# Performance work log

Hardware: AMD Instinct MI355X
Metric: run time of the kernel (lower is better)

The kernel has to match this reference:

```python
import jax, jax.numpy as jnp
import numpy as np

N = 50000      # nodes
E = 800000     # edges (avg degree 16)
F_IN = 128     # num_node_features
D = 64         # embedding_size (= per-head out_channels)
H = 4          # heads
ED = 20        # edge_dim (hardcoded in module)
SLOPE = 0.2    # GATv2 leaky_relu negative slope
N_LAYERS = 3   # conv applied 3 times with shared weights


def setup_inputs() -> dict:
    key = jax.random.key(0)
    ks = jax.random.split(key, 12)
    s = 0.1
    return {
        "x": jax.random.normal(ks[0], (N, F_IN), jnp.float32),
        "edge_attr": jax.random.normal(ks[1], (E, 2), jnp.float32),
        "edge_index": jax.random.randint(ks[2], (2, E), 0, N, dtype=jnp.int32),
        # f: Linear(F_IN, D)
        "f_W": jax.random.normal(ks[3], (F_IN, D), jnp.float32) * s,
        "f_b": jnp.zeros((D,), jnp.float32),
        # fe: Linear(2, ED)
        "fe_W": jax.random.normal(ks[4], (2, ED), jnp.float32) * s,
        "fe_b": jnp.zeros((ED,), jnp.float32),
        # GATv2Conv lin_l / lin_r: Linear(D, H*D)
        "Wl": jax.random.normal(ks[5], (D, H * D), jnp.float32) * s,
        "bl": jnp.zeros((H * D,), jnp.float32),
        "Wr": jax.random.normal(ks[6], (D, H * D), jnp.float32) * s,
        "br": jnp.zeros((H * D,), jnp.float32),
        # lin_edge: Linear(ED, H*D, bias=False)
        "We": jax.random.normal(ks[7], (ED, H * D), jnp.float32) * s,
        # attention vector att: [H, D]
        "att": jax.random.normal(ks[8], (H, D), jnp.float32) * s,
        # final bias (concat=False -> size D)
        "bias": jnp.zeros((D,), jnp.float32),
    }


def _gatv2_conv(h, e_emb, src, dst, Wl, bl, Wr, br, We, att, bias):
    # h: [N, D], e_emb: [E, ED], src/dst: [E]
    xl = (h @ Wl + bl).reshape(-1, H, D)        # source transform  [N,H,D]
    xr = (h @ Wr + br).reshape(-1, H, D)        # target transform  [N,H,D]
    ee = (e_emb @ We).reshape(-1, H, D)         # edge transform    [E,H,D]
    m = jax.nn.leaky_relu(xl[src] + xr[dst] + ee, SLOPE)  # [E,H,D]
    score = jnp.einsum('ehd,hd->eh', m, att)    # [E,H]
    # segment softmax over incoming edges of each dst node
    smax = jax.ops.segment_max(score, dst, num_segments=N)   # [N,H]
    ex = jnp.exp(score - smax[dst])
    denom = jax.ops.segment_sum(ex, dst, num_segments=N)     # [N,H]
    alpha = ex / denom[dst]                                  # [E,H]
    out = jax.ops.segment_sum(alpha[:, :, None] * xl[src], dst, num_segments=N)  # [N,H,D]
    return out.mean(axis=1) + bias              # concat=False -> head mean, [N,D]


def reference(x, edge_attr, edge_index, f_W, f_b, fe_W, fe_b, Wl, bl, Wr, br, We, att, bias):
    src, dst = edge_index[0], edge_index[1]
    h = jax.nn.relu(x @ f_W + f_b)
    e = jax.nn.relu(edge_attr @ fe_W + fe_b)
    for _ in range(N_LAYERS):
        h = jax.nn.relu(_gatv2_conv(h, e, src, dst, Wl, bl, Wr, br, We, att, bias))
    return h
```

## Files before the change

kernel.cpp:

```cpp
#include <hip/hip_runtime.h>
#include <math.h>

typedef float v2f __attribute__((ext_vector_type(2)));

#define LN2_INV 1.4426950408889634f

__device__ __forceinline__ float fexp2(float x) {
#if __has_builtin(__builtin_amdgcn_exp2f)
    return __builtin_amdgcn_exp2f(x);
#else
    return exp2f(x);
#endif
}

__device__ __forceinline__ int rdlane_i(int v, int k) {
    return __builtin_amdgcn_readlane(v, k);
}

__device__ __forceinline__ v2f max2(v2f a, float b) {
    v2f r; r.x = fmaxf(a.x, b); r.y = fmaxf(a.y, b); return r;
}
__device__ __forceinline__ v2f min2(v2f a, float b) {
    v2f r; r.x = fminf(a.x, b); r.y = fminf(a.y, b); return r;
}

#define DPP_ROW_ADD(V, CTRL) \
    V += __int_as_float(__builtin_amdgcn_update_dpp(0, __float_as_int(V), CTRL, 0xf, 0xf, true));

__global__ __launch_bounds__(256) void k_h0(const float* __restrict__ x,
                                            const float* __restrict__ fW,
                                            const float* __restrict__ fb,
                                            float* __restrict__ h0) {
    __shared__ __align__(16) float xs[8 * 128];
    int t = threadIdx.x;
    int base = blockIdx.x * 8;
#pragma unroll
    for (int r = 0; r < 4; ++r) { int j = r * 256 + t; xs[j] = x[base * 128 + j]; }
    __syncthreads();
    int c = t & 63, half = t >> 6;
    float acc0 = fb[c], acc1 = fb[c];
    int m0 = half, m1 = half + 4;
#pragma unroll 8
    for (int k0 = 0; k0 < 128; k0 += 4) {
        float4 a = *(const float4*)&xs[m0 * 128 + k0];
        float4 b = *(const float4*)&xs[m1 * 128 + k0];
        float w0 = fW[(k0 + 0) * 64 + c], w1 = fW[(k0 + 1) * 64 + c];
        float w2 = fW[(k0 + 2) * 64 + c], w3 = fW[(k0 + 3) * 64 + c];
        acc0 = fmaf(a.x, w0, fmaf(a.y, w1, fmaf(a.z, w2, fmaf(a.w, w3, acc0))));
        acc1 = fmaf(b.x, w0, fmaf(b.y, w1, fmaf(b.z, w2, fmaf(b.w, w3, acc1))));
    }
    h0[(base + m0) * 64 + c] = fmaxf(acc0, 0.f);
    h0[(base + m1) * 64 + c] = fmaxf(acc1, 0.f);
}

__global__ __launch_bounds__(256) void k_xlxr(const float* __restrict__ h,
                                              const float* __restrict__ Wl,
                                              const float* __restrict__ Wr,
                                              const float* __restrict__ bl,
                                              const float* __restrict__ br,
                                              float* __restrict__ xl,
                                              float* __restrict__ xr) {
    __shared__ __align__(16) float hs[16 * 64];
    int t = threadIdx.x;
    int base = blockIdx.x * 16;
#pragma unroll
    for (int r = 0; r < 4; ++r) hs[r * 256 + t] = h[base * 64 + r * 256 + t];
    __syncthreads();
    float bL = bl[t], bR = br[t];
    float accl[16], accr[16];
#pragma unroll
    for (int m = 0; m < 16; ++m) { accl[m] = bL; accr[m] = bR; }
#pragma unroll 4
    for (int k0 = 0; k0 < 64; k0 += 4) {
        float wl[4], wr[4];
#pragma unroll
        for (int q = 0; q < 4; ++q) {
            wl[q] = Wl[(k0 + q) * 256 + t];
            wr[q] = Wr[(k0 + q) * 256 + t];
        }
#pragma unroll
        for (int m = 0; m < 16; ++m) {
            float4 hv = *(const float4*)&hs[m * 64 + k0];
            accl[m] = fmaf(hv.x, wl[0], fmaf(hv.y, wl[1], fmaf(hv.z, wl[2], fmaf(hv.w, wl[3], accl[m]))));
            accr[m] = fmaf(hv.x, wr[0], fmaf(hv.y, wr[1], fmaf(hv.z, wr[2], fmaf(hv.w, wr[3], accr[m]))));
        }
    }
#pragma unroll
    for (int m = 0; m < 16; ++m) {
        xl[(base + m) * 256 + t] = accl[m];
        xr[(base + m) * 256 + t] = accr[m];
    }
}

__global__ void k_zero(int* __restrict__ deg, int* __restrict__ counter, int Nn) {
    int i = blockIdx.x * 256 + threadIdx.x;
    if (i < Nn) deg[i] = 0;
    if (i == 0) *counter = 0;
}

__global__ void k_count(const int* __restrict__ dstArr, int* __restrict__ deg, int Ee) {
    int e = blockIdx.x * 256 + threadIdx.x;
    if (e < Ee) atomicAdd(&deg[dstArr[e]], 1);
}

__global__ void k_alloc(const int* __restrict__ deg, int* __restrict__ counter,
                        int* __restrict__ start, int* __restrict__ cursor, int Nn) {
    int n = blockIdx.x * 256 + threadIdx.x;
    if (n < Nn) {
        int d = deg[n];
        int b = atomicAdd(counter, d);
        start[n] = b;
        cursor[n] = b;
    }
}

__global__ void k_fill(const int* __restrict__ dstArr, const int* __restrict__ srcArr,
                       const float* __restrict__ eattr, const float* __restrict__ feW,
                       const float* __restrict__ feb, int* __restrict__ cursor,
                       int* __restrict__ rec, int Ee) {
    int e = blockIdx.x * 256 + threadIdx.x;
    if (e >= Ee) return;
    float a0 = eattr[2 * e], a1 = eattr[2 * e + 1];
    int p = atomicAdd(&cursor[dstArr[e]], 1);
    float* r = (float*)(rec + (size_t)p * 24);
    float s[20];
#pragma unroll
    for (int k = 0; k < 20; ++k)
        s[k] = fmaxf(fmaf(a0, feW[k], fmaf(a1, feW[20 + k], feb[k])), 0.f);
#pragma unroll
    for (int j = 0; j < 5; ++j)
        ((float4*)r)[j] = make_float4(s[4 * j], s[4 * j + 1], s[4 * j + 2], s[4 * j + 3]);
    ((int*)r)[20] = srcArr[e];
}

__global__ __launch_bounds__(256, 3) void k_edge(
    const float4* __restrict__ xl4p, const float4* __restrict__ xr4p,
    const float* __restrict__ att, const float4* __restrict__ We4,
    const int* __restrict__ rec, const int* __restrict__ start,
    const int* __restrict__ deg, const float* __restrict__ bias,
    float* __restrict__ hout, int Nn) {
    const int lane = threadIdx.x & 63;
    const int n = (int)((blockIdx.x * 256u + threadIdx.x) >> 6);
    if (n >= Nn) return;

    const int dn = __builtin_amdgcn_readfirstlane(deg[n]);
    float4 bias4 = ((const float4*)bias)[lane & 15];
    if (dn == 0) {
        if (lane < 16) {
            float4 o = make_float4(fmaxf(bias4.x, 0.f), fmaxf(bias4.y, 0.f),
                                   fmaxf(bias4.z, 0.f), fmaxf(bias4.w, 0.f));
            ((float4*)hout)[(size_t)n * 16 + lane] = o;
        }
        return;
    }
    const int s0 = __builtin_amdgcn_readfirstlane(start[n]);
    const int* rb = rec + (size_t)s0 * 24 + (lane & 31);

    float4 attv = ((const float4*)att)[lane];
    v2f att01 = {attv.x * LN2_INV, attv.y * LN2_INV};
    v2f att23 = {attv.z * LN2_INV, attv.w * LN2_INV};
    v2f at201 = 0.2f * att01, at223 = 0.2f * att23;
    float4 xrv = xr4p[(size_t)n * 64 + lane];
    v2f xr01 = {xrv.x, xrv.y}, xr23 = {xrv.z, xrv.w};
    v2f we01[20], we23[20];
#pragma unroll
    for (int k = 0; k < 20; ++k) {
        float4 w = We4[k * 64 + lane];
        we01[k].x = w.x; we01[k].y = w.y;
        we23[k].x = w.z; we23[k].y = w.w;
    }
    const int bperm = ((lane & 48) | 15) << 2;

    v2f acc01 = {0.f, 0.f}, acc23 = {0.f, 0.f};
    float l = 0.f;

    int i1 = dn > 1 ? 1 : 0;
    int i2p = dn > 2 ? 2 : (dn - 1);
    int rv0 = rb[0];
    int rv1 = rb[(size_t)i1 * 24];
    int rv2 = rb[(size_t)i2p * 24];
    int src0 = rdlane_i(rv0, 20);
    float4 xl0 = xl4p[(size_t)src0 * 64 + lane];
    int src1 = rdlane_i(rv1, 20);
    float4 xl1 = xl4p[(size_t)src1 * 64 + lane];

    for (int i = 0; i < dn; ++i) {
        int i3 = (i + 3 < dn) ? (i + 3) : (dn - 1);
        int rvN = rb[(size_t)i3 * 24];
        int src2 = rdlane_i(rv2, 20);
        float4 xl2 = xl4p[(size_t)src2 * 64 + lane];

        v2f xl01 = {xl0.x, xl0.y}, xl23 = {xl0.z, xl0.w};

        v2f ea01, ea23, eb01, eb23;
        {
            float sa = __int_as_float(rdlane_i(rv0, 0));
            float sb = __int_as_float(rdlane_i(rv0, 1));
            ea01 = sa * we01[0];  ea23 = sa * we23[0];
            eb01 = sb * we01[1];  eb23 = sb * we23[1];
        }
#pragma unroll
        for (int k = 2; k < 20; k += 2) {
            float sa = __int_as_float(rdlane_i(rv0, k));
            float sb = __int_as_float(rdlane_i(rv0, k + 1));
            ea01 += sa * we01[k];      ea23 += sa * we23[k];
            eb01 += sb * we01[k + 1];  eb23 += sb * we23[k + 1];
        }
        v2f ee01 = ea01 + eb01;
        v2f ee23 = ea23 + eb23;

        v2f v01 = (xl01 + xr01) + ee01;
        v2f v23 = (xl23 + xr23) + ee23;
        v2f p01 = att01 * max2(v01, 0.f) + at201 * min2(v01, 0.f);
        v2f p23 = att23 * max2(v23, 0.f) + at223 * min2(v23, 0.f);
        v2f pr = p01 + p23;
        float ps = pr.x + pr.y;
        DPP_ROW_ADD(ps, 0x111)
        DPP_ROW_ADD(ps, 0x112)
        DPP_ROW_ADD(ps, 0x114)
        DPP_ROW_ADD(ps, 0x118)
        float sc = __int_as_float(
            __builtin_amdgcn_ds_bpermute(bperm, __float_as_int(ps)));
        float w_ = fexp2(sc);
        l += w_;
        acc01 += w_ * xl01;
        acc23 += w_ * xl23;

        rv0 = rv1; rv1 = rv2; rv2 = rvN;
        xl0 = xl1; xl1 = xl2;
    }

    float inv = 0.25f / l;
    float4 r = make_float4(acc01.x * inv, acc01.y * inv, acc23.x * inv, acc23.y * inv);
    r.x += __shfl_xor(r.x, 16, 64); r.x += __shfl_xor(r.x, 32, 64);
    r.y += __shfl_xor(r.y, 16, 64); r.y += __shfl_xor(r.y, 32, 64);
    r.z += __shfl_xor(r.z, 16, 64); r.z += __shfl_xor(r.z, 32, 64);
    r.w += __shfl_xor(r.w, 16, 64); r.w += __shfl_xor(r.w, 32, 64);
    if (lane < 16) {
        float4 o = make_float4(fmaxf(r.x + bias4.x, 0.f), fmaxf(r.y + bias4.y, 0.f),
                               fmaxf(r.z + bias4.z, 0.f), fmaxf(r.w + bias4.w, 0.f));
        ((float4*)hout)[(size_t)n * 16 + lane] = o;
    }
}

extern "C" void kernel_launch(void* const* d_in, const int* in_sizes, int n_in,
                              void* d_out, int out_size, void* d_ws, size_t ws_size,
                              hipStream_t stream) {
    const float* x     = (const float*)d_in[0];
    const float* eattr = (const float*)d_in[1];
    const int*   eidx  = (const int*)d_in[2];
    const float* fW    = (const float*)d_in[3];
    const float* fb    = (const float*)d_in[4];
    const float* feW   = (const float*)d_in[5];
    const float* feb   = (const float*)d_in[6];
    const float* Wl    = (const float*)d_in[7];
    const float* bl    = (const float*)d_in[8];
    const float* Wr    = (const float*)d_in[9];
    const float* br    = (const float*)d_in[10];
    const float* We    = (const float*)d_in[11];
    const float* att   = (const float*)d_in[12];
    const float* bias  = (const float*)d_in[13];
    float* out = (float*)d_out;

    const int N = in_sizes[0] / 128;
    const int E = in_sizes[1] / 2;
    const int* srcArr = eidx;
    const int* dstArr = eidx + E;

    char* p = (char*)d_ws;
    auto alloc = [&](size_t bytes) -> char* {
        char* r = p;
        p += (bytes + 255) & ~(size_t)255;
        return r;
    };
    float* hA   = (float*)alloc((size_t)N * 64 * 4);
    float* hB   = (float*)alloc((size_t)N * 64 * 4);
    float* xl   = (float*)alloc((size_t)N * 256 * 4);
    float* xr   = (float*)alloc((size_t)N * 256 * 4);
    int* deg    = (int*)alloc((size_t)N * 4);
    int* start  = (int*)alloc((size_t)N * 4);
    int* cursor = (int*)alloc((size_t)N * 4);
    int* counter = (int*)alloc(256);
    int* rec    = (int*)alloc((size_t)E * 24 * 4);

    k_h0<<<N / 8, 256, 0, stream>>>(x, fW, fb, hA);
    k_zero<<<(N + 255) / 256, 256, 0, stream>>>(deg, counter, N);
    k_count<<<(E + 255) / 256, 256, 0, stream>>>(dstArr, deg, E);
    k_alloc<<<(N + 255) / 256, 256, 0, stream>>>(deg, counter, start, cursor, N);
    k_fill<<<(E + 255) / 256, 256, 0, stream>>>(dstArr, srcArr, eattr, feW, feb,
                                                cursor, rec, E);

    const float* hin = hA;
    for (int layer = 0; layer < 3; ++layer) {
        float* hout = (layer == 2) ? out : ((layer == 0) ? hB : hA);
        k_xlxr<<<N / 16, 256, 0, stream>>>(hin, Wl, Wr, bl, br, xl, xr);
        k_edge<<<(N * 64) / 256, 256, 0, stream>>>(
            (const float4*)xl, (const float4*)xr, att, (const float4*)We,
            rec, start, deg, bias, hout, N);
        hin = hout;
    }
}
```

Measured before the change: 903.8 us.

## Split each node's edge loop across two wavefronts with scalar record loads

```diff
diff --git a/kernel.cpp b/kernel.cpp
--- a/kernel.cpp
+++ b/kernel.cpp
@@ -1,7 +1,5 @@
 #include <hip/hip_runtime.h>
 #include <math.h>
-
-typedef float v2f __attribute__((ext_vector_type(2)));
 
 #define LN2_INV 1.4426950408889634f
 
@@ -11,17 +9,6 @@
 #else
     return exp2f(x);
 #endif
-}
-
-__device__ __forceinline__ int rdlane_i(int v, int k) {
-    return __builtin_amdgcn_readlane(v, k);
-}
-
-__device__ __forceinline__ v2f max2(v2f a, float b) {
-    v2f r; r.x = fmaxf(a.x, b); r.y = fmaxf(a.y, b); return r;
-}
-__device__ __forceinline__ v2f min2(v2f a, float b) {
-    v2f r; r.x = fminf(a.x, b); r.y = fminf(a.y, b); return r;
 }
 
 #define DPP_ROW_ADD(V, CTRL) \
@@ -133,113 +120,118 @@
     ((int*)r)[20] = srcArr[e];
 }
 
-__global__ __launch_bounds__(256, 3) void k_edge(
-    const float4* __restrict__ xl4p, const float4* __restrict__ xr4p,
-    const float* __restrict__ att, const float4* __restrict__ We4,
+#define LOADREC(e, S, SRC) do {                                          \
+    size_t _b = (size_t)(e) * 24;                                        \
+    _Pragma("unroll")                                                    \
+    for (int _k = 0; _k < 20; ++_k) S[_k] = rfb[_b + _k];                \
+    SRC = rib[_b + 20];                                                  \
+} while (0)
+
+#define EDGE_BODY(S, XLV) do {                                           \
+    float _e0a = S[0] * we2[0].x, _e1a = S[0] * we2[0].y;                \
+    float _e0b = S[1] * we2[1].x, _e1b = S[1] * we2[1].y;                \
+    _Pragma("unroll")                                                    \
+    for (int _k = 2; _k < 20; _k += 2) {                                 \
+        _e0a = fmaf(S[_k], we2[_k].x, _e0a);                             \
+        _e1a = fmaf(S[_k], we2[_k].y, _e1a);                             \
+        _e0b = fmaf(S[_k + 1], we2[_k + 1].x, _e0b);                     \
+        _e1b = fmaf(S[_k + 1], we2[_k + 1].y, _e1b);                     \
+    }                                                                    \
+    float _v0 = (XLV.x + xrv.x) + (_e0a + _e0b);                         \
+    float _v1 = (XLV.y + xrv.y) + (_e1a + _e1b);                         \
+    float _m0 = fmaxf(_v0, 0.2f * _v0);                                  \
+    float _m1 = fmaxf(_v1, 0.2f * _v1);                                  \
+    float _ps = fmaf(attv.x, _m0, attv.y * _m1);                         \
+    DPP_ROW_ADD(_ps, 0x111)                                              \
+    DPP_ROW_ADD(_ps, 0x112)                                              \
+    DPP_ROW_ADD(_ps, 0x114)                                              \
+    DPP_ROW_ADD(_ps, 0x118)                                              \
+    DPP_ROW_ADD(_ps, 0x142)                                              \
+    float _sc = __int_as_float(                                          \
+        __builtin_amdgcn_ds_swizzle(__float_as_int(_ps), 0x03E0));       \
+    float _w = fexp2(_sc);                                               \
+    l += _w;                                                             \
+    acc.x = fmaf(_w, XLV.x, acc.x);                                      \
+    acc.y = fmaf(_w, XLV.y, acc.y);                                      \
+} while (0)
+
+__global__ __launch_bounds__(128, 4) void k_edge(
+    const float2* __restrict__ xl2p, const float2* __restrict__ xr2p,
+    const float* __restrict__ att, const float2* __restrict__ We2p,
     const int* __restrict__ rec, const int* __restrict__ start,
     const int* __restrict__ deg, const float* __restrict__ bias,
     float* __restrict__ hout, int Nn) {
+    const int wid = threadIdx.x >> 6;
     const int lane = threadIdx.x & 63;
-    const int n = (int)((blockIdx.x * 256u + threadIdx.x) >> 6);
-    if (n >= Nn) return;
+    const int n = blockIdx.x;
 
     const int dn = __builtin_amdgcn_readfirstlane(deg[n]);
-    float4 bias4 = ((const float4*)bias)[lane & 15];
     if (dn == 0) {
-        if (lane < 16) {
-            float4 o = make_float4(fmaxf(bias4.x, 0.f), fmaxf(bias4.y, 0.f),
-                                   fmaxf(bias4.z, 0.f), fmaxf(bias4.w, 0.f));
-            ((float4*)hout)[(size_t)n * 16 + lane] = o;
+        if (threadIdx.x < 32) {
+            float2 b2 = ((const float2*)bias)[threadIdx.x];
+            ((float2*)hout)[(size_t)n * 32 + threadIdx.x] =
+                make_float2(fmaxf(b2.x, 0.f), fmaxf(b2.y, 0.f));
         }
         return;
     }
     const int s0 = __builtin_amdgcn_readfirstlane(start[n]);
-    const int* rb = rec + (size_t)s0 * 24 + (lane & 31);
-
-    float4 attv = ((const float4*)att)[lane];
-    v2f att01 = {attv.x * LN2_INV, attv.y * LN2_INV};
-    v2f att23 = {attv.z * LN2_INV, attv.w * LN2_INV};
-    v2f at201 = 0.2f * att01, at223 = 0.2f * att23;
-    float4 xrv = xr4p[(size_t)n * 64 + lane];
-    v2f xr01 = {xrv.x, xrv.y}, xr23 = {xrv.z, xrv.w};
-    v2f we01[20], we23[20];
-#pragma unroll
-    for (int k = 0; k < 20; ++k) {
-        float4 w = We4[k * 64 + lane];
-        we01[k].x = w.x; we01[k].y = w.y;
-        we23[k].x = w.z; we23[k].y = w.w;
-    }
-    const int bperm = ((lane & 48) | 15) << 2;
-
-    v2f acc01 = {0.f, 0.f}, acc23 = {0.f, 0.f};
+    const float* rfb = (const float*)rec + (size_t)s0 * 24;
+    const int* rib = rec + (size_t)s0 * 24;
+
+    const float2* xw = xl2p + (size_t)wid * 64;
+
+    float2 xrv = xr2p[(size_t)n * 128 + wid * 64 + lane];
+    float2 attv = ((const float2*)att)[wid * 64 + lane];
+    attv.x *= LN2_INV; attv.y *= LN2_INV;
+    float2 we2[20];
+#pragma unroll
+    for (int k = 0; k < 20; ++k) we2[k] = We2p[k * 128 + wid * 64 + lane];
+
+    float2 acc = make_float2(0.f, 0.f);
     float l = 0.f;
 
-    int i1 = dn > 1 ? 1 : 0;
-    int i2p = dn > 2 ? 2 : (dn - 1);
-    int rv0 = rb[0];
-    int rv1 = rb[(size_t)i1 * 24];
-    int rv2 = rb[(size_t)i2p * 24];
-    int src0 = rdlane_i(rv0, 20);
-    float4 xl0 = xl4p[(size_t)src0 * 64 + lane];
-    int src1 = rdlane_i(rv1, 20);
-    float4 xl1 = xl4p[(size_t)src1 * 64 + lane];
-
-    for (int i = 0; i < dn; ++i) {
-        int i3 = (i + 3 < dn) ? (i + 3) : (dn - 1);
-        int rvN = rb[(size_t)i3 * 24];
-        int src2 = rdlane_i(rv2, 20);
-        float4 xl2 = xl4p[(size_t)src2 * 64 + lane];
-
-        v2f xl01 = {xl0.x, xl0.y}, xl23 = {xl0.z, xl0.w};
-
-        v2f ea01, ea23, eb01, eb23;
+    float sA[20], sB[20];
+    int srcA, srcB;
+    float2 xlA, xlB;
+
+    LOADREC(0, sA, srcA);
+    xlA = xw[(size_t)srcA * 128 + lane];
+    if (dn > 1) {
+        LOADREC(1, sB, srcB);
+        xlB = xw[(size_t)srcB * 128 + lane];
+    }
+
+    int i = 0;
+    for (; i + 2 <= dn; i += 2) {
+        EDGE_BODY(sA, xlA);
         {
-            float sa = __int_as_float(rdlane_i(rv0, 0));
-            float sb = __int_as_float(rdlane_i(rv0, 1));
-            ea01 = sa * we01[0];  ea23 = sa * we23[0];
-            eb01 = sb * we01[1];  eb23 = sb * we23[1];
-        }
-#pragma unroll
-        for (int k = 2; k < 20; k += 2) {
-            float sa = __int_as_float(rdlane_i(rv0, k));
-            float sb = __int_as_float(rdlane_i(rv0, k + 1));
-            ea01 += sa * we01[k];      ea23 += sa * we23[k];
-            eb01 += sb * we01[k + 1];  eb23 += sb * we23[k + 1];
-        }
-        v2f ee01 = ea01 + eb01;
-        v2f ee23 = ea23 + eb23;
-
-        v2f v01 = (xl01 + xr01) + ee01;
-        v2f v23 = (xl23 + xr23) + ee23;
-        v2f p01 = att01 * max2(v01, 0.f) + at201 * min2(v01, 0.f);
-        v2f p23 = att23 * max2(v23, 0.f) + at223 * min2(v23, 0.f);
-        v2f pr = p01 + p23;
-        float ps = pr.x + pr.y;
-        DPP_ROW_ADD(ps, 0x111)
-        DPP_ROW_ADD(ps, 0x112)
-        DPP_ROW_ADD(ps, 0x114)
-        DPP_ROW_ADD(ps, 0x118)
-        float sc = __int_as_float(
-            __builtin_amdgcn_ds_bpermute(bperm, __float_as_int(ps)));
-        float w_ = fexp2(sc);
-        l += w_;
-        acc01 += w_ * xl01;
-        acc23 += w_ * xl23;
-
-        rv0 = rv1; rv1 = rv2; rv2 = rvN;
-        xl0 = xl1; xl1 = xl2;
-    }
-
-    float inv = 0.25f / l;
-    float4 r = make_float4(acc01.x * inv, acc01.y * inv, acc23.x * inv, acc23.y * inv);
-    r.x += __shfl_xor(r.x, 16, 64); r.x += __shfl_xor(r.x, 32, 64);
-    r.y += __shfl_xor(r.y, 16, 64); r.y += __shfl_xor(r.y, 32, 64);
-    r.z += __shfl_xor(r.z, 16, 64); r.z += __shfl_xor(r.z, 32, 64);
-    r.w += __shfl_xor(r.w, 16, 64); r.w += __shfl_xor(r.w, 32, 64);
-    if (lane < 16) {
-        float4 o = make_float4(fmaxf(r.x + bias4.x, 0.f), fmaxf(r.y + bias4.y, 0.f),
-                               fmaxf(r.z + bias4.z, 0.f), fmaxf(r.w + bias4.w, 0.f));
-        ((float4*)hout)[(size_t)n * 16 + lane] = o;
+            int e = (i + 2 < dn) ? (i + 2) : (dn - 1);
+            LOADREC(e, sA, srcA);
+            xlA = xw[(size_t)srcA * 128 + lane];
+        }
+        EDGE_BODY(sB, xlB);
+        {
+            int e = (i + 3 < dn) ? (i + 3) : (dn - 1);
+            LOADREC(e, sB, srcB);
+            xlB = xw[(size_t)srcB * 128 + lane];
+        }
+    }
+    if (i < dn) EDGE_BODY(sA, xlA);
+
+    float invl = 1.0f / l;
+    float p0 = acc.x * invl, p1 = acc.y * invl;
+    p0 += __shfl_xor(p0, 32, 64);
+    p1 += __shfl_xor(p1, 32, 64);
+
+    __shared__ float2 comb[32];
+    if (wid == 1 && lane < 32) comb[lane] = make_float2(p0, p1);
+    __syncthreads();
+    if (wid == 0 && lane < 32) {
+        float2 q = comb[lane];
+        float2 b2 = ((const float2*)bias)[lane];
+        float r0 = fmaxf(fmaf(0.25f, p0 + q.x, b2.x), 0.f);
+        float r1 = fmaxf(fmaf(0.25f, p1 + q.y, b2.y), 0.f);
+        ((float2*)hout)[(size_t)n * 32 + lane] = make_float2(r0, r1);
     }
 }
 
@@ -294,8 +286,8 @@
     for (int layer = 0; layer < 3; ++layer) {
         float* hout = (layer == 2) ? out : ((layer == 0) ? hB : hA);
         k_xlxr<<<N / 16, 256, 0, stream>>>(hin, Wl, Wr, bl, br, xl, xr);
-        k_edge<<<(N * 64) / 256, 256, 0, stream>>>(
-            (const float4*)xl, (const float4*)xr, att, (const float4*)We,
+        k_edge<<<N, 128, 0, stream>>>(
+            (const float2*)xl, (const float2*)xr, att, (const float2*)We,
             rec, start, deg, bias, hout, N);
         hin = hout;
     }
```

Result: slower. 1.086 ms (+20.1%).

## Stage edge features through LDS, use packed FP32 math, double-buffer edge loop

Applied to the files above, without the earlier changes.

```diff
diff --git a/kernel.cpp b/kernel.cpp
--- a/kernel.cpp
+++ b/kernel.cpp
@@ -15,6 +15,21 @@
 
 __device__ __forceinline__ int rdlane_i(int v, int k) {
     return __builtin_amdgcn_readlane(v, k);
+}
+
+__device__ __forceinline__ v2f pk_fma(v2f a, v2f b, v2f c) {
+    asm("v_pk_fma_f32 %0, %1, %2, %0" : "+v"(c) : "v"(a), "v"(b));
+    return c;
+}
+__device__ __forceinline__ v2f pk_add(v2f a, v2f b) {
+    v2f d;
+    asm("v_pk_add_f32 %0, %1, %2" : "=v"(d) : "v"(a), "v"(b));
+    return d;
+}
+__device__ __forceinline__ v2f pk_mul(v2f a, v2f b) {
+    v2f d;
+    asm("v_pk_mul_f32 %0, %1, %2" : "=v"(d) : "v"(a), "v"(b));
+    return d;
 }
 
 __device__ __forceinline__ v2f max2(v2f a, float b) {
@@ -92,10 +107,12 @@
     }
 }
 
-__global__ void k_zero(int* __restrict__ deg, int* __restrict__ counter, int Nn) {
+__global__ void k_zero(int* __restrict__ deg, int* __restrict__ counter,
+                       int* __restrict__ rec, int Nn, int Ee) {
     int i = blockIdx.x * 256 + threadIdx.x;
     if (i < Nn) deg[i] = 0;
     if (i == 0) *counter = 0;
+    if (blockIdx.x == 0 && threadIdx.x < 96) rec[(size_t)Ee * 24 + threadIdx.x] = 0;
 }
 
 __global__ void k_count(const int* __restrict__ dstArr, int* __restrict__ deg, int Ee) {
@@ -133,6 +150,46 @@
     ((int*)r)[20] = srcArr[e];
 }
 
+#define COMPUTE_EDGE(Sp, XL) do {                                            \
+    v2f xl01 = {XL.x, XL.y}, xl23 = {XL.z, XL.w};                            \
+    v2f sa = *(const v2f*)&Sp[0];                                            \
+    v2f ea01 = pk_mul(sa, we01[0]);  v2f ea23 = pk_mul(sa, we23[0]);         \
+    v2f sb = *(const v2f*)&Sp[2];                                            \
+    v2f eb01 = pk_mul(sb, we01[1]);  v2f eb23 = pk_mul(sb, we23[1]);         \
+    _Pragma("unroll")                                                        \
+    for (int k = 2; k < 20; k += 2) {                                        \
+        v2f ka = *(const v2f*)&Sp[2 * k];                                    \
+        v2f kb = *(const v2f*)&Sp[2 * k + 2];                                \
+        ea01 = pk_fma(ka, we01[k], ea01);                                    \
+        ea23 = pk_fma(ka, we23[k], ea23);                                    \
+        eb01 = pk_fma(kb, we01[k + 1], eb01);                                \
+        eb23 = pk_fma(kb, we23[k + 1], eb23);                                \
+    }                                                                        \
+    v2f v01 = pk_add(pk_add(xl01, xr01), pk_add(ea01, eb01));                \
+    v2f v23 = pk_add(pk_add(xl23, xr23), pk_add(ea23, eb23));                \
+    v2f p01 = pk_fma(at201, min2(v01, 0.f), pk_mul(att01, max2(v01, 0.f))); \
+    v2f p23 = pk_fma(at223, min2(v23, 0.f), pk_mul(att23, max2(v23, 0.f))); \
+    v2f pr = pk_add(p01, p23);                                               \
+    float ps = pr.x + pr.y;                                                  \
+    DPP_ROW_ADD(ps, 0x111)                                                   \
+    DPP_ROW_ADD(ps, 0x112)                                                   \
+    DPP_ROW_ADD(ps, 0x114)                                                   \
+    DPP_ROW_ADD(ps, 0x118)                                                   \
+    float sc = __int_as_float(                                               \
+        __builtin_amdgcn_ds_bpermute(bperm, __float_as_int(ps)));            \
+    float w_ = fexp2(sc);                                                    \
+    l += w_;                                                                 \
+    v2f w2 = {w_, w_};                                                       \
+    acc01 = pk_fma(w2, xl01, acc01);                                         \
+    acc23 = pk_fma(w2, xl23, acc23);                                         \
+} while (0)
+
+#define STAGE(Sp, RV) do {                                                   \
+    float _f = __int_as_float(RV);                                           \
+    v2f _p = {_f, _f};                                                       \
+    *(v2f*)&Sp[2 * lane] = _p;                                               \
+} while (0)
+
 __global__ __launch_bounds__(256, 3) void k_edge(
     const float4* __restrict__ xl4p, const float4* __restrict__ xr4p,
     const float* __restrict__ att, const float4* __restrict__ We4,
@@ -140,8 +197,10 @@
     const int* __restrict__ deg, const float* __restrict__ bias,
     float* __restrict__ hout, int Nn) {
     const int lane = threadIdx.x & 63;
+    const int wv = threadIdx.x >> 6;
     const int n = (int)((blockIdx.x * 256u + threadIdx.x) >> 6);
     if (n >= Nn) return;
+    __shared__ __align__(16) float sbuf[4][2][128];
 
     const int dn = __builtin_amdgcn_readfirstlane(deg[n]);
     float4 bias4 = ((const float4*)bias)[lane & 15];
@@ -170,65 +229,41 @@
         we23[k].x = w.z; we23[k].y = w.w;
     }
     const int bperm = ((lane & 48) | 15) << 2;
+    float* sA = &sbuf[wv][0][0];
+    float* sB = &sbuf[wv][1][0];
 
     v2f acc01 = {0.f, 0.f}, acc23 = {0.f, 0.f};
     float l = 0.f;
 
-    int i1 = dn > 1 ? 1 : 0;
-    int i2p = dn > 2 ? 2 : (dn - 1);
-    int rv0 = rb[0];
-    int rv1 = rb[(size_t)i1 * 24];
-    int rv2 = rb[(size_t)i2p * 24];
-    int src0 = rdlane_i(rv0, 20);
-    float4 xl0 = xl4p[(size_t)src0 * 64 + lane];
-    int src1 = rdlane_i(rv1, 20);
-    float4 xl1 = xl4p[(size_t)src1 * 64 + lane];
-
-    for (int i = 0; i < dn; ++i) {
-        int i3 = (i + 3 < dn) ? (i + 3) : (dn - 1);
-        int rvN = rb[(size_t)i3 * 24];
-        int src2 = rdlane_i(rv2, 20);
-        float4 xl2 = xl4p[(size_t)src2 * 64 + lane];
-
-        v2f xl01 = {xl0.x, xl0.y}, xl23 = {xl0.z, xl0.w};
-
-        v2f ea01, ea23, eb01, eb23;
+    int rvA = rb[0];
+    int rvB = rb[24];
+    int rvA2 = rb[48];
+    int rvB2 = rb[72];
+    STAGE(sA, rvA);
+    STAGE(sB, rvB);
+    int srcA = rdlane_i(rvA, 20);
+    int srcB = rdlane_i(rvB, 20);
+    float4 xlA = xl4p[(unsigned)(srcA * 64 + lane)];
+    float4 xlB = xl4p[(unsigned)(srcB * 64 + lane)];
+
+    const int nfull = dn >> 1;
+    for (int t = 0; t < nfull; ++t) {
+        COMPUTE_EDGE(sA, xlA);
+        STAGE(sA, rvA2);
         {
-            float sa = __int_as_float(rdlane_i(rv0, 0));
-            float sb = __int_as_float(rdlane_i(rv0, 1));
-            ea01 = sa * we01[0];  ea23 = sa * we23[0];
-            eb01 = sb * we01[1];  eb23 = sb * we23[1];
-        }
-#pragma unroll
-        for (int k = 2; k < 20; k += 2) {
-            float sa = __int_as_float(rdlane_i(rv0, k));
-            float sb = __int_as_float(rdlane_i(rv0, k + 1));
-            ea01 += sa * we01[k];      ea23 += sa * we23[k];
-            eb01 += sb * we01[k + 1];  eb23 += sb * we23[k + 1];
-        }
-        v2f ee01 = ea01 + eb01;
-        v2f ee23 = ea23 + eb23;
-
-        v2f v01 = (xl01 + xr01) + ee01;
-        v2f v23 = (xl23 + xr23) + ee23;
-        v2f p01 = att01 * max2(v01, 0.f) + at201 * min2(v01, 0.f);
-        v2f p23 = att23 * max2(v23, 0.f) + at223 * min2(v23, 0.f);
-        v2f pr = p01 + p23;
-        float ps = pr.x + pr.y;
-        DPP_ROW_ADD(ps, 0x111)
-        DPP_ROW_ADD(ps, 0x112)
-        DPP_ROW_ADD(ps, 0x114)
-        DPP_ROW_ADD(ps, 0x118)
-        float sc = __int_as_float(
-            __builtin_amdgcn_ds_bpermute(bperm, __float_as_int(ps)));
-        float w_ = fexp2(sc);
-        l += w_;
-        acc01 += w_ * xl01;
-        acc23 += w_ * xl23;
-
-        rv0 = rv1; rv1 = rv2; rv2 = rvN;
-        xl0 = xl1; xl1 = xl2;
-    }
+            int srcN = rdlane_i(rvA2, 20);
+            xlA = xl4p[(unsigned)(srcN * 64 + lane)];
+            rvA2 = rb[(2 * t + 4) * 24];
+        }
+        COMPUTE_EDGE(sB, xlB);
+        STAGE(sB, rvB2);
+        {
+            int srcN = rdlane_i(rvB2, 20);
+            xlB = xl4p[(unsigned)(srcN * 64 + lane)];
+            rvB2 = rb[(2 * t + 5) * 24];
+        }
+    }
+    if (dn & 1) COMPUTE_EDGE(sA, xlA);
 
     float inv = 0.25f / l;
     float4 r = make_float4(acc01.x * inv, acc01.y * inv, acc23.x * inv, acc23.y * inv);
@@ -281,10 +316,10 @@
     int* start  = (int*)alloc((size_t)N * 4);
     int* cursor = (int*)alloc((size_t)N * 4);
     int* counter = (int*)alloc(256);
-    int* rec    = (int*)alloc((size_t)E * 24 * 4);
+    int* rec    = (int*)alloc((size_t)(E + 4) * 24 * 4);
 
     k_h0<<<N / 8, 256, 0, stream>>>(x, fW, fb, hA);
-    k_zero<<<(N + 255) / 256, 256, 0, stream>>>(deg, counter, N);
+    k_zero<<<(N + 255) / 256, 256, 0, stream>>>(deg, counter, rec, N, E);
     k_count<<<(E + 255) / 256, 256, 0, stream>>>(dstArr, deg, E);
     k_alloc<<<(N + 255) / 256, 256, 0, stream>>>(deg, counter, start, cursor, N);
     k_fill<<<(E + 255) / 256, 256, 0, stream>>>(dstArr, srcArr, eattr, feW, feb,
```

After: 1.268 ms. 40.3% more time.

## Use scalar edge-record loads and packed FMAs in two-stream pipelined edge loop

Applied to the files above, without the earlier changes.

```diff
diff --git a/kernel.cpp b/kernel.cpp
--- a/kernel.cpp
+++ b/kernel.cpp
@@ -13,15 +13,18 @@
 #endif
 }
 
-__device__ __forceinline__ int rdlane_i(int v, int k) {
-    return __builtin_amdgcn_readlane(v, k);
-}
-
-__device__ __forceinline__ v2f max2(v2f a, float b) {
-    v2f r; r.x = fmaxf(a.x, b); r.y = fmaxf(a.y, b); return r;
-}
-__device__ __forceinline__ v2f min2(v2f a, float b) {
-    v2f r; r.x = fminf(a.x, b); r.y = fminf(a.y, b); return r;
+__device__ __forceinline__ v2f pk_fma(v2f a, v2f b, v2f c) {
+    asm("v_pk_fma_f32 %0, %1, %2, %0" : "+v"(c) : "v"(a), "v"(b));
+    return c;
+}
+__device__ __forceinline__ v2f pk_fma_s(v2f a_s, v2f b, v2f c) {
+    asm("v_pk_fma_f32 %0, %1, %2, %0" : "+v"(c) : "s"(a_s), "v"(b));
+    return c;
+}
+__device__ __forceinline__ v2f pk_mul_s(v2f a_s, v2f b) {
+    v2f d;
+    asm("v_pk_mul_f32 %0, %1, %2" : "=v"(d) : "s"(a_s), "v"(b));
+    return d;
 }
 
 #define DPP_ROW_ADD(V, CTRL) \
@@ -92,10 +95,12 @@
     }
 }
 
-__global__ void k_zero(int* __restrict__ deg, int* __restrict__ counter, int Nn) {
+__global__ void k_zero(int* __restrict__ deg, int* __restrict__ counter,
+                       int* __restrict__ rec, int Nn, int Ee) {
     int i = blockIdx.x * 256 + threadIdx.x;
     if (i < Nn) deg[i] = 0;
     if (i == 0) *counter = 0;
+    if (blockIdx.x == 0 && threadIdx.x < 96) rec[(size_t)Ee * 24 + threadIdx.x] = 0;
 }
 
 __global__ void k_count(const int* __restrict__ dstArr, int* __restrict__ deg, int Ee) {
@@ -133,6 +138,49 @@
     ((int*)r)[20] = srcArr[e];
 }
 
+#define LOAD_BLOCK(SK, E_) do {                                              \
+    const float* _rp = rf + (size_t)(E_) * 24;                               \
+    _Pragma("unroll")                                                        \
+    for (int _k = 0; _k < 20; ++_k) SK[_k] = _rp[_k];                        \
+} while (0)
+
+#define COMPUTE_EDGE(SK, XL) do {                                            \
+    v2f _sp0 = {SK[0], SK[1]};                                               \
+    v2f _a0 = pk_mul_s(_sp0, weI0[0]);                                       \
+    v2f _a1 = pk_mul_s(_sp0, weI1[0]);                                       \
+    v2f _a2 = pk_mul_s(_sp0, weI2[0]);                                       \
+    v2f _a3 = pk_mul_s(_sp0, weI3[0]);                                       \
+    _Pragma("unroll")                                                        \
+    for (int _p = 1; _p < 10; ++_p) {                                        \
+        v2f _s = {SK[2 * _p], SK[2 * _p + 1]};                               \
+        _a0 = pk_fma_s(_s, weI0[_p], _a0);                                   \
+        _a1 = pk_fma_s(_s, weI1[_p], _a1);                                   \
+        _a2 = pk_fma_s(_s, weI2[_p], _a2);                                   \
+        _a3 = pk_fma_s(_s, weI3[_p], _a3);                                   \
+    }                                                                        \
+    float _v0 = (XL.x + xrv.x) + (_a0.x + _a0.y);                            \
+    float _v1 = (XL.y + xrv.y) + (_a1.x + _a1.y);                            \
+    float _v2 = (XL.z + xrv.z) + (_a2.x + _a2.y);                            \
+    float _v3 = (XL.w + xrv.w) + (_a3.x + _a3.y);                            \
+    float _m0 = fmaxf(_v0, 0.2f * _v0);                                      \
+    float _m1 = fmaxf(_v1, 0.2f * _v1);                                      \
+    float _m2 = fmaxf(_v2, 0.2f * _v2);                                      \
+    float _m3 = fmaxf(_v3, 0.2f * _v3);                                      \
+    float _ps = fmaf(at0, _m0, fmaf(at1, _m1, fmaf(at2, _m2, at3 * _m3)));   \
+    DPP_ROW_ADD(_ps, 0x111)                                                  \
+    DPP_ROW_ADD(_ps, 0x112)                                                  \
+    DPP_ROW_ADD(_ps, 0x114)                                                  \
+    DPP_ROW_ADD(_ps, 0x118)                                                  \
+    float _sc = __int_as_float(                                              \
+        __builtin_amdgcn_ds_bpermute(bperm, __float_as_int(_ps)));           \
+    float _w = fexp2(_sc);                                                   \
+    l += _w;                                                                 \
+    v2f _w2 = {_w, _w};                                                      \
+    v2f _xl01 = {XL.x, XL.y}, _xl23 = {XL.z, XL.w};                          \
+    acc01 = pk_fma(_w2, _xl01, acc01);                                       \
+    acc23 = pk_fma(_w2, _xl23, acc23);                                       \
+} while (0)
+
 __global__ __launch_bounds__(256, 3) void k_edge(
     const float4* __restrict__ xl4p, const float4* __restrict__ xr4p,
     const float* __restrict__ att, const float4* __restrict__ We4,
@@ -154,81 +202,52 @@
         return;
     }
     const int s0 = __builtin_amdgcn_readfirstlane(start[n]);
-    const int* rb = rec + (size_t)s0 * 24 + (lane & 31);
+    const float* rf = (const float*)rec + (size_t)s0 * 24;
+    const int* ri = rec + (size_t)s0 * 24;
 
     float4 attv = ((const float4*)att)[lane];
-    v2f att01 = {attv.x * LN2_INV, attv.y * LN2_INV};
-    v2f att23 = {attv.z * LN2_INV, attv.w * LN2_INV};
-    v2f at201 = 0.2f * att01, at223 = 0.2f * att23;
+    float at0 = attv.x * LN2_INV, at1 = attv.y * LN2_INV;
+    float at2 = attv.z * LN2_INV, at3 = attv.w * LN2_INV;
     float4 xrv = xr4p[(size_t)n * 64 + lane];
-    v2f xr01 = {xrv.x, xrv.y}, xr23 = {xrv.z, xrv.w};
-    v2f we01[20], we23[20];
-#pragma unroll
-    for (int k = 0; k < 20; ++k) {
-        float4 w = We4[k * 64 + lane];
-        we01[k].x = w.x; we01[k].y = w.y;
-        we23[k].x = w.z; we23[k].y = w.w;
+    v2f weI0[10], weI1[10], weI2[10], weI3[10];
+#pragma unroll
+    for (int p = 0; p < 10; ++p) {
+        float4 w0 = We4[(2 * p) * 64 + lane];
+        float4 w1 = We4[(2 * p + 1) * 64 + lane];
+        weI0[p].x = w0.x; weI0[p].y = w1.x;
+        weI1[p].x = w0.y; weI1[p].y = w1.y;
+        weI2[p].x = w0.z; weI2[p].y = w1.z;
+        weI3[p].x = w0.w; weI3[p].y = w1.w;
     }
     const int bperm = ((lane & 48) | 15) << 2;
 
     v2f acc01 = {0.f, 0.f}, acc23 = {0.f, 0.f};
     float l = 0.f;
 
-    int i1 = dn > 1 ? 1 : 0;
-    int i2p = dn > 2 ? 2 : (dn - 1);
-    int rv0 = rb[0];
-    int rv1 = rb[(size_t)i1 * 24];
-    int rv2 = rb[(size_t)i2p * 24];
-    int src0 = rdlane_i(rv0, 20);
-    float4 xl0 = xl4p[(size_t)src0 * 64 + lane];
-    int src1 = rdlane_i(rv1, 20);
-    float4 xl1 = xl4p[(size_t)src1 * 64 + lane];
-
-    for (int i = 0; i < dn; ++i) {
-        int i3 = (i + 3 < dn) ? (i + 3) : (dn - 1);
-        int rvN = rb[(size_t)i3 * 24];
-        int src2 = rdlane_i(rv2, 20);
-        float4 xl2 = xl4p[(size_t)src2 * 64 + lane];
-
-        v2f xl01 = {xl0.x, xl0.y}, xl23 = {xl0.z, xl0.w};
-
-        v2f ea01, ea23, eb01, eb23;
-        {
-            float sa = __int_as_float(rdlane_i(rv0, 0));
-            float sb = __int_as_float(rdlane_i(rv0, 1));
-            ea01 = sa * we01[0];  ea23 = sa * we23[0];
-            eb01 = sb * we01[1];  eb23 = sb * we23[1];
-        }
-#pragma unroll
-        for (int k = 2; k < 20; k += 2) {
-            float sa = __int_as_float(rdlane_i(rv0, k));
-            float sb = __int_as_float(rdlane_i(rv0, k + 1));
-            ea01 += sa * we01[k];      ea23 += sa * we23[k];
-            eb01 += sb * we01[k + 1];  eb23 += sb * we23[k + 1];
-        }
-        v2f ee01 = ea01 + eb01;
-        v2f ee23 = ea23 + eb23;
-
-        v2f v01 = (xl01 + xr01) + ee01;
-        v2f v23 = (xl23 + xr23) + ee23;
-        v2f p01 = att01 * max2(v01, 0.f) + at201 * min2(v01, 0.f);
-        v2f p23 = att23 * max2(v23, 0.f) + at223 * min2(v23, 0.f);
-        v2f pr = p01 + p23;
-        float ps = pr.x + pr.y;
-        DPP_ROW_ADD(ps, 0x111)
-        DPP_ROW_ADD(ps, 0x112)
-        DPP_ROW_ADD(ps, 0x114)
-        DPP_ROW_ADD(ps, 0x118)
-        float sc = __int_as_float(
-            __builtin_amdgcn_ds_bpermute(bperm, __float_as_int(ps)));
-        float w_ = fexp2(sc);
-        l += w_;
-        acc01 += w_ * xl01;
-        acc23 += w_ * xl23;
-
-        rv0 = rv1; rv1 = rv2; rv2 = rvN;
-        xl0 = xl1; xl1 = xl2;
-    }
+    float skA[20], skB[20];
+    LOAD_BLOCK(skA, 0);
+    LOAD_BLOCK(skB, 1);
+    int sA0 = ri[20];
+    int sB0 = ri[44];
+    float4 xlA = xl4p[(size_t)(unsigned)sA0 * 64 + lane];
+    float4 xlB = xl4p[(size_t)(unsigned)sB0 * 64 + lane];
+    int srcA = ri[2 * 24 + 20];
+    int srcB = ri[3 * 24 + 20];
+
+    const int nfull = dn >> 1;
+    for (int t = 0; t < nfull; ++t) {
+        float4 xlA2 = xl4p[(size_t)(unsigned)srcA * 64 + lane];
+        srcA = ri[(size_t)(2 * t + 4) * 24 + 20];
+        COMPUTE_EDGE(skA, xlA);
+        LOAD_BLOCK(skA, 2 * t + 2);
+        xlA = xlA2;
+        float4 xlB2 = xl4p[(size_t)(unsigned)srcB * 64 + lane];
+        srcB = ri[(size_t)(2 * t + 5) * 24 + 20];
+        COMPUTE_EDGE(skB, xlB);
+        LOAD_BLOCK(skB, 2 * t + 3);
+        xlB = xlB2;
+    }
+    if (dn & 1) COMPUTE_EDGE(skA, xlA);
 
     float inv = 0.25f / l;
     float4 r = make_float4(acc01.x * inv, acc01.y * inv, acc23.x * inv, acc23.y * inv);
@@ -281,10 +300,10 @@
     int* start  = (int*)alloc((size_t)N * 4);
     int* cursor = (int*)alloc((size_t)N * 4);
     int* counter = (int*)alloc(256);
-    int* rec    = (int*)alloc((size_t)E * 24 * 4);
+    int* rec    = (int*)alloc((size_t)(E + 4) * 24 * 4);
 
     k_h0<<<N / 8, 256, 0, stream>>>(x, fW, fb, hA);
-    k_zero<<<(N + 255) / 256, 256, 0, stream>>>(deg, counter, N);
+    k_zero<<<(N + 255) / 256, 256, 0, stream>>>(deg, counter, rec, N, E);
     k_count<<<(E + 255) / 256, 256, 0, stream>>>(dstArr, deg, E);
     k_alloc<<<(N + 255) / 256, 256, 0, stream>>>(deg, counter, start, cursor, N);
     k_fill<<<(E + 255) / 256, 256, 0, stream>>>(dstArr, srcArr, eattr, feW, feb,
```

Result: slower. 967.2 us (+7.0%).
